# Performance work log

Hardware: AMD Instinct MI355X
Metric: run time of the kernel (lower is better)

The kernel has to match this reference:

```python
import jax, jax.numpy as jnp
from jax import lax
import numpy as np

RADIUS = 0.1
NSAMPLE = 32
STRIDE = 4
NUM_DIR = 32
BN_EPS = 1e-5


def _fps(p, m):
    # furthest point sampling: p (B,N,3) -> (B,m) int32 indices, start at index 0
    B, N, _ = p.shape

    def step(carry, _):
        dists, last = carry
        lp = jnp.take_along_axis(p, jnp.broadcast_to(last[:, None, None], (B, 1, 3)), axis=1)
        d = jnp.sum((p - lp) ** 2, axis=-1)
        dists = jnp.minimum(dists, d)
        nxt = jnp.argmax(dists, axis=-1).astype(jnp.int32)
        return (dists, nxt), nxt

    last0 = jnp.zeros((B,), jnp.int32)
    d0 = jnp.full((B, N), 1e10, p.dtype)
    _, rest = lax.scan(step, (d0, last0), None, length=m - 1)
    return jnp.concatenate([last0[None, :], rest], axis=0).T  # (B, m)


def _ball_query(q, p, k, radius):
    # q (B,M,3) centers, p (B,N,3) support -> (B,M,k) indices of first k points in ball,
    # padded with the first found index (PointNet++ convention)
    N = p.shape[1]
    d2 = jnp.sum((q[:, :, None, :] - p[:, None, :, :]) ** 2, axis=-1)  # (B,M,N)
    cand = jnp.where(d2 < radius * radius, jnp.arange(N, dtype=jnp.int32), N)
    cand = jnp.sort(cand, axis=-1)[:, :, :k]
    first = cand[:, :, :1]
    return jnp.where(cand == N, first, cand)


def _bn(x, g, b, m, v):
    # BatchNorm1d eval mode on (B,C,N)
    return (x - m[:, None]) * (g[:, None] / jnp.sqrt(v[:, None] + BN_EPS)) + b[:, None]


def _normalize(x, axis):
    return x / jnp.maximum(jnp.linalg.norm(x, axis=axis, keepdims=True), 1e-12)


def setup_inputs() -> dict:
    key = jax.random.key(0)
    ks = jax.random.split(key, 16)
    B, N, Cin, Cout = 4, 8192, 128, 256
    half = Cout // 2
    s = 0.02
    return {
        "p": jax.random.uniform(ks[0], (B, N, 3), jnp.float32),
        "f": jax.random.normal(ks[1], (B, Cin, N), jnp.float32),
        "conv1_w": jax.random.normal(ks[2], (Cout, Cin), jnp.float32) * s,
        "conv1_b": jax.random.normal(ks[3], (Cout,), jnp.float32) * s,
        "skip_w": jax.random.normal(ks[4], (Cout, Cin), jnp.float32) * s,
        "skip_b": jax.random.normal(ks[5], (Cout,), jnp.float32) * s,
        "bn1_g": jnp.ones((Cout,), jnp.float32),
        "bn1_b": jnp.zeros((Cout,), jnp.float32),
        "bn1_m": jax.random.normal(ks[6], (Cout,), jnp.float32) * 0.1,
        "bn1_v": jax.random.uniform(ks[7], (Cout,), jnp.float32) + 0.5,
        "dir_vectors": jax.random.normal(ks[8], (NUM_DIR, 3), jnp.float32),
        "de_w1": jax.random.normal(ks[9], (half, NUM_DIR), jnp.float32) * s,
        "de_g": jnp.ones((half,), jnp.float32),
        "de_bb": jnp.zeros((half,), jnp.float32),
        "de_m": jax.random.normal(ks[10], (half,), jnp.float32) * 0.1,
        "de_v": jax.random.uniform(ks[11], (half,), jnp.float32) + 0.5,
        "de_w2": jax.random.normal(ks[12], (Cout, half), jnp.float32) * s,
        "de_b2": jax.random.normal(ks[13], (Cout,), jnp.float32) * s,
    }


def reference(p, f, conv1_w, conv1_b, skip_w, skip_b, bn1_g, bn1_b, bn1_m, bn1_v,
              dir_vectors, de_w1, de_g, de_bb, de_m, de_v, de_w2, de_b2):
    B, N, _ = p.shape
    Cout = conv1_w.shape[0]
    M, K = N // STRIDE, NSAMPLE

    # FPS sampling + centroid gather
    idx = _fps(p, M)  # (B,M)
    new_p = jnp.take_along_axis(p, jnp.broadcast_to(idx[:, :, None], (B, M, 3)), axis=1)

    # residual branch: gather input feats at centroids, 1x1 conv (bn_after=False)
    fi = jnp.take_along_axis(f, jnp.broadcast_to(idx[:, None, :], (B, f.shape[1], M)), axis=2)
    identity = jnp.einsum('oc,bcm->bom', skip_w, fi) + skip_b[:, None]

    # convs1: 1x1 conv on all N points
    f1 = jnp.einsum('oc,bcn->bon', conv1_w, f) + conv1_b[:, None]  # (B,Cout,N)

    # ball-query grouping
    qidx = _ball_query(new_p, p, K, RADIUS)  # (B,M,K)
    idxf = qidx.reshape(B, M * K)
    gp = jnp.take_along_axis(p, jnp.broadcast_to(idxf[:, :, None], (B, M * K, 3)), axis=1).reshape(B, M, K, 3)
    dp = jnp.transpose(gp - new_p[:, :, None, :], (0, 3, 1, 2))  # (B,3,M,K)
    fj = jnp.take_along_axis(f1, jnp.broadcast_to(idxf[:, None, :], (B, Cout, M * K)), axis=2).reshape(B, Cout, M, K)

    # directional encoding
    dpn = _normalize(dp, axis=1)
    vec = _normalize(dir_vectors, axis=1)  # (NUM_DIR,3)
    theta = jnp.einsum('md,bdnk->bmnk', vec, dpn)  # (B,NUM_DIR,M,K)
    tmax = theta.max(axis=-1)  # (B,NUM_DIR,M)
    h = jnp.einsum('om,bmn->bon', de_w1, tmax)
    h = jax.nn.gelu(_bn(h, de_g, de_bb, de_m, de_v), approximate=False)
    pe = jnp.einsum('oc,bcn->bon', de_w2, h) + de_b2[:, None]

    # neighbor max-pool + BN + residuals
    f_out = _bn(fj.max(axis=-1), bn1_g, bn1_b, bn1_m, bn1_v) + pe + identity
    return new_p, f_out
```

## Files before the change

kernel.cpp:

```cpp
#include <hip/hip_runtime.h>

#define BATCH 4
#define NPTS 8192
#define MPTS 2048
#define CIN 128
#define CO 256
#define KS 32
#define ND 32
#define HALF 128

typedef unsigned int u32;
typedef unsigned long long u64;
typedef float f32x2 __attribute__((ext_vector_type(2)));

#define DPPC_QUAD_XOR1 0xB1
#define DPPC_QUAD_XOR2 0x4E
#define DPPC_ROW_MIRROR 0x140
#define DPPC_ROW_HALF_MIRROR 0x141
#define DPPC_ROW_BCAST15 0x142
#define DPPC_ROW_BCAST31 0x143

template<int CTRL>
__device__ __forceinline__ float dpp_max(float v) {
    int o = __builtin_amdgcn_update_dpp(__float_as_int(-1e30f), __float_as_int(v),
                                        CTRL, 0xF, 0xF, false);
    return fmaxf(v, __int_as_float(o));
}
__device__ __forceinline__ float wave_max_f32(float v) {
    v = dpp_max<DPPC_QUAD_XOR1>(v);
    v = dpp_max<DPPC_QUAD_XOR2>(v);
    v = dpp_max<DPPC_ROW_HALF_MIRROR>(v);
    v = dpp_max<DPPC_ROW_MIRROR>(v);
    v = dpp_max<DPPC_ROW_BCAST15>(v);
    v = dpp_max<DPPC_ROW_BCAST31>(v);
    return __int_as_float(__builtin_amdgcn_readlane(__float_as_int(v), 63));
}

__device__ __forceinline__ f32x2 pk_add(f32x2 a, f32x2 b) {
    f32x2 r;
    asm("v_pk_add_f32 %0, %1, %2" : "=v"(r) : "v"(a), "v"(b));
    return r;
}
__device__ __forceinline__ f32x2 pk_mul(f32x2 a, f32x2 b) {
    f32x2 r;
    asm("v_pk_mul_f32 %0, %1, %2" : "=v"(r) : "v"(a), "v"(b));
    return r;
}

struct FeatSmem {
    float sdx[KS], sdy[KS], sdz[KS];
    float ltm[ND], lfi[CIN], lh[HALF];
    int swidx[4][KS];
    int scnt[4];
    int nb[KS], nbp[KS];
};

__global__
__attribute__((amdgpu_flat_work_group_size(512, 512), amdgpu_waves_per_eu(2, 2)))
void k_mega(
    const float* __restrict__ p, const float* __restrict__ f,
    const float* __restrict__ conv1_w, const float* __restrict__ conv1_b,
    const float* __restrict__ skip_w,  const float* __restrict__ skip_b,
    const float* __restrict__ bn1_g, const float* __restrict__ bn1_b,
    const float* __restrict__ bn1_m, const float* __restrict__ bn1_v,
    const float* __restrict__ dirv,  const float* __restrict__ de_w1,
    const float* __restrict__ de_g,  const float* __restrict__ de_bb,
    const float* __restrict__ de_m,  const float* __restrict__ de_v,
    const float* __restrict__ de_w2, const float* __restrict__ de_b2,
    float* __restrict__ out_newp, float* __restrict__ out_f,
    int* __restrict__ idx, float* __restrict__ f1t,
    int* prog, int* f1all) {
    __shared__ __align__(16) char smem_u[16640];
    if (blockIdx.x < 4) {
        u64*    wkey = (u64*)smem_u;
        float4* wxyz = (float4*)(smem_u + 128);
        int b = blockIdx.x, t = threadIdx.x;
        int lane = t & 63, wid = t >> 6;
        int j0 = t * 16;
        const float* pb = p + (size_t)b * NPTS * 3;
        const float* pt = pb + t * 48;
        float px[16], py[16], pz[16];
#pragma unroll
        for (int c = 0; c < 4; ++c) {
            float4 q0 = *(const float4*)(pt + c * 12 + 0);
            float4 q1 = *(const float4*)(pt + c * 12 + 4);
            float4 q2 = *(const float4*)(pt + c * 12 + 8);
            px[c*4+0] = q0.x; py[c*4+0] = q0.y; pz[c*4+0] = q0.z;
            px[c*4+1] = q0.w; py[c*4+1] = q1.x; pz[c*4+1] = q1.y;
            px[c*4+2] = q1.z; py[c*4+2] = q1.w; pz[c*4+2] = q2.x;
            px[c*4+3] = q2.y; py[c*4+3] = q2.z; pz[c*4+3] = q2.w;
        }
        f32x2 px2[8], py2[8], pz2[8], dist2[8];
#pragma unroll
        for (int i = 0; i < 8; ++i) {
            px2[i].x = px[2*i]; px2[i].y = px[2*i+1];
            py2[i].x = py[2*i]; py2[i].y = py[2*i+1];
            pz2[i].x = pz[2*i]; pz2[i].y = pz[2*i+1];
        }
#pragma unroll
        for (int i = 0; i < 8; ++i) {
            asm volatile("" : "+v"(px2[i]), "+v"(py2[i]), "+v"(pz2[i]));
        }
#pragma unroll
        for (int i = 0; i < 8; ++i) { dist2[i].x = 1e10f; dist2[i].y = 1e10f; }
        float lx = pb[0], ly = pb[1], lz = pb[2];
        if (t == 0) {
            out_newp[(size_t)b * MPTS * 3 + 0] = lx;
            out_newp[(size_t)b * MPTS * 3 + 1] = ly;
            out_newp[(size_t)b * MPTS * 3 + 2] = lz;
            __hip_atomic_store(idx + b * MPTS, 0, __ATOMIC_RELAXED,
                               __HIP_MEMORY_SCOPE_AGENT);
        }
        for (int s = 1; s < MPTS; ++s) {
            int par = s & 1;
            f32x2 nlx2, nly2, nlz2;
            nlx2.x = -lx; nlx2.y = -lx;
            nly2.x = -ly; nly2.y = -ly;
            nlz2.x = -lz; nlz2.y = -lz;
            float bv = -1e30f; int bi = 0;
            float bx = px2[0].x, by = py2[0].x, bz = pz2[0].x;
#pragma unroll
            for (int i = 0; i < 8; ++i) {
                f32x2 dx = pk_add(px2[i], nlx2);
                f32x2 dy = pk_add(py2[i], nly2);
                f32x2 dz = pk_add(pz2[i], nlz2);
                f32x2 d  = pk_add(pk_add(pk_mul(dx, dx), pk_mul(dy, dy)),
                                  pk_mul(dz, dz));
                float nd0 = fminf(dist2[i].x, d.x);
                float nd1 = fminf(dist2[i].y, d.y);
                dist2[i].x = nd0;
                dist2[i].y = nd1;
                bool g0 = nd0 > bv;
                bi = g0 ? 2*i : bi;
                bx = g0 ? px2[i].x : bx;
                by = g0 ? py2[i].x : by;
                bz = g0 ? pz2[i].x : bz;
                bv = fmaxf(bv, nd0);
                bool g1 = nd1 > bv;
                bi = g1 ? 2*i+1 : bi;
                bx = g1 ? px2[i].y : bx;
                by = g1 ? py2[i].y : by;
                bz = g1 ? pz2[i].y : bz;
                bv = fmaxf(bv, nd1);
            }
            float gmw = wave_max_f32(bv);
            u64 mask = __ballot(bv == gmw);
            int first = __ffsll((long long)mask) - 1;
            if (lane == first) {
                wkey[par * 8 + wid] = ((u64)__float_as_uint(gmw) << 32)
                                    | (u64)(u32)(NPTS - 1 - (j0 + bi));
                wxyz[par * 8 + wid] = make_float4(bx, by, bz, 0.0f);
            }
            __syncthreads();
            const u64* wk = wkey + par * 8;
            u64 k0 = wk[0], k1 = wk[1], k2 = wk[2], k3 = wk[3];
            u64 k4 = wk[4], k5 = wk[5], k6 = wk[6], k7 = wk[7];
            u64 m01 = k1 > k0 ? k1 : k0;  int w01 = k1 > k0 ? 1 : 0;
            u64 m23 = k3 > k2 ? k3 : k2;  int w23 = k3 > k2 ? 3 : 2;
            u64 m45 = k5 > k4 ? k5 : k4;  int w45 = k5 > k4 ? 5 : 4;
            u64 m67 = k7 > k6 ? k7 : k6;  int w67 = k7 > k6 ? 7 : 6;
            u64 m03 = m23 > m01 ? m23 : m01; int w03 = m23 > m01 ? w23 : w01;
            u64 m47 = m67 > m45 ? m67 : m45; int w47 = m67 > m45 ? w67 : w45;
            u64 best = m47 > m03 ? m47 : m03; int ww = m47 > m03 ? w47 : w03;
            float4 wp = wxyz[par * 8 + ww];
            lx = wp.x; ly = wp.y; lz = wp.z;
            if (t == 0) {
                int w0 = (NPTS - 1 - (int)(best & 0xFFFFFFFFull)) & (NPTS - 1);
                asm volatile("s_waitcnt vmcnt(0)" ::: "memory");
                __hip_atomic_store(prog + b, s, __ATOMIC_RELAXED,
                                   __HIP_MEMORY_SCOPE_AGENT);
                out_newp[((size_t)b * MPTS + s) * 3 + 0] = lx;
                out_newp[((size_t)b * MPTS + s) * 3 + 1] = ly;
                out_newp[((size_t)b * MPTS + s) * 3 + 2] = lz;
                __hip_atomic_store(idx + b * MPTS + s, w0, __ATOMIC_RELAXED,
                                   __HIP_MEMORY_SCOPE_AGENT);
            }
        }
        if (t == 0) {
            asm volatile("s_waitcnt vmcnt(0)" ::: "memory");
            __hip_atomic_store(prog + b, MPTS, __ATOMIC_RELAXED,
                               __HIP_MEMORY_SCOPE_AGENT);
        }
    } else if (blockIdx.x < 4 + 1024) {
        float* fT = (float*)smem_u;
        int blk = blockIdx.x - 4;
        int b = blk >> 8;
        int n0 = (blk & 255) << 5;
        int t = threadIdx.x;
        const float* fb = f + (size_t)b * CIN * NPTS;
        for (int e = t; e < CIN * 32; e += 512) {
            int k = e >> 5, j = e & 31;
            fT[e] = fb[(size_t)k * NPTS + n0 + j];
        }
        __syncthreads();
        int c = t & 255, jh = (t >> 8) << 4;
        float bias = conv1_b[c];
        float acc[16];
#pragma unroll
        for (int j = 0; j < 16; ++j) acc[j] = bias;
        const float4* wrow4 = (const float4*)(conv1_w + (size_t)c * CIN);
        const float4* fT4 = (const float4*)fT;
        for (int k4 = 0; k4 < 32; ++k4) {
            float4 wv = wrow4[k4];
#pragma unroll
            for (int sub = 0; sub < 4; ++sub) {
                float w = sub == 0 ? wv.x : sub == 1 ? wv.y : sub == 2 ? wv.z : wv.w;
                int k = k4 * 4 + sub;
                int base = (k * 32 + jh) >> 2;
                float4 a0 = fT4[base+0], a1 = fT4[base+1], a2 = fT4[base+2], a3 = fT4[base+3];
                acc[0]  = fmaf(w, a0.x, acc[0]);  acc[1]  = fmaf(w, a0.y, acc[1]);
                acc[2]  = fmaf(w, a0.z, acc[2]);  acc[3]  = fmaf(w, a0.w, acc[3]);
                acc[4]  = fmaf(w, a1.x, acc[4]);  acc[5]  = fmaf(w, a1.y, acc[5]);
                acc[6]  = fmaf(w, a1.z, acc[6]);  acc[7]  = fmaf(w, a1.w, acc[7]);
                acc[8]  = fmaf(w, a2.x, acc[8]);  acc[9]  = fmaf(w, a2.y, acc[9]);
                acc[10] = fmaf(w, a2.z, acc[10]); acc[11] = fmaf(w, a2.w, acc[11]);
                acc[12] = fmaf(w, a3.x, acc[12]); acc[13] = fmaf(w, a3.y, acc[13]);
                acc[14] = fmaf(w, a3.z, acc[14]); acc[15] = fmaf(w, a3.w, acc[15]);
            }
        }
        float* dst = f1t + ((size_t)b * NPTS + n0 + jh) * CO + c;
#pragma unroll
        for (int j = 0; j < 16; ++j) dst[(size_t)j * CO] = acc[j];
        __syncthreads();
        if (t == 0) {
            __threadfence();
            atomicAdd(f1all, 1);
        }
    } else {
        int fb = (int)blockIdx.x - (4 + 1024);
        int m  = fb >> 1;
        int bA = (fb & 1) * 2;
        int t = threadIdx.x;
        if (t == 0) {
            int need = m + 1;
            for (int it = 0; it < (1 << 21); ++it) {
                if (__hip_atomic_load(prog + bA, __ATOMIC_RELAXED,
                                      __HIP_MEMORY_SCOPE_AGENT) >= need) break;
                __builtin_amdgcn_s_sleep(127);
            }
            for (int it = 0; it < (1 << 21); ++it) {
                if (__hip_atomic_load(prog + bA + 1, __ATOMIC_RELAXED,
                                      __HIP_MEMORY_SCOPE_AGENT) >= need) break;
                __builtin_amdgcn_s_sleep(127);
            }
            for (int it = 0; it < (1 << 21); ++it) {
                if (__hip_atomic_load(f1all, __ATOMIC_RELAXED,
                                      __HIP_MEMORY_SCOPE_AGENT) >= 1024) break;
                __builtin_amdgcn_s_sleep(127);
            }
            (void)__hip_atomic_load(prog + bA, __ATOMIC_ACQUIRE,
                                    __HIP_MEMORY_SCOPE_AGENT);
        }
        __syncthreads();
        int qi = t >> 8;
        int tq = t & 255;
        int b  = bA + qi;
        FeatSmem* fs = ((FeatSmem*)smem_u) + qi;
        int lane = t & 63, wq = (t >> 6) & 3;
        const float* pb = p + (size_t)b * NPTS * 3;
        int i0 = idx[(size_t)b * MPTS + m] & (NPTS - 1);
        float qx = pb[i0 * 3 + 0], qy = pb[i0 * 3 + 1], qz = pb[i0 * 3 + 2];
        const float R2 = 0.1f * 0.1f;

        int cnt = 0;
        int seg = wq * 2048;
        for (int base = 0; base < 2048; base += 64) {
            int j = seg + base + lane;
            float dx = __fsub_rn(pb[j * 3 + 0], qx);
            float dy = __fsub_rn(pb[j * 3 + 1], qy);
            float dz = __fsub_rn(pb[j * 3 + 2], qz);
            float d2 = __fadd_rn(__fadd_rn(__fmul_rn(dx, dx), __fmul_rn(dy, dy)),
                                 __fmul_rn(dz, dz));
            bool hit = d2 < R2;
            u64 mask = __ballot(hit);
            if (hit) {
                int pos = cnt + __popcll(mask & ((1ull << lane) - 1ull));
                if (pos < KS) fs->swidx[wq][pos] = j;
            }
            cnt += __popcll(mask);
            if (cnt >= KS) break;
        }
        if (lane == 0) fs->scnt[wq] = cnt < KS ? cnt : KS;
        __syncthreads();
        int c0s = fs->scnt[0], c1s = fs->scnt[1], c2s = fs->scnt[2], c3s = fs->scnt[3];
        int st1 = c0s, st2 = c0s + c1s, st3 = c0s + c1s + c2s;
        int total = c0s + c1s + c2s + c3s; if (total > KS) total = KS;
        if (total < 1) total = 1;
        if (tq < 128) {
            int ww = tq >> 5, l = tq & 31;
            int stw = (ww == 0) ? 0 : (ww == 1) ? st1 : (ww == 2) ? st2 : st3;
            int cw  = (ww == 0) ? c0s : (ww == 1) ? c1s : (ww == 2) ? c2s : c3s;
            int gp = stw + l;
            if (l < cw && gp < KS) fs->nb[gp] = fs->swidx[ww][l];
        }
        __syncthreads();
        if (tq < KS) {
            int jk = fs->nb[tq < total ? tq : 0] & (NPTS - 1);
            fs->nbp[tq] = jk;
            float dx = pb[jk * 3 + 0] - qx;
            float dy = pb[jk * 3 + 1] - qy;
            float dz = pb[jk * 3 + 2] - qz;
            float nr = fmaxf(sqrtf(dx * dx + dy * dy + dz * dz), 1e-12f);
            fs->sdx[tq] = dx / nr; fs->sdy[tq] = dy / nr; fs->sdz[tq] = dz / nr;
        }
        if (tq >= 128) {
            fs->lfi[tq - 128] = f[((size_t)b * CIN + (tq - 128)) * NPTS + i0];
        }
        __syncthreads();
        if (tq < ND) {
            float ax = dirv[tq * 3], ay = dirv[tq * 3 + 1], az = dirv[tq * 3 + 2];
            float n = fmaxf(sqrtf(ax * ax + ay * ay + az * az), 1e-12f);
            float vx = ax / n, vy = ay / n, vz = az / n;
            float tm = -1e30f;
#pragma unroll
            for (int k = 0; k < KS; ++k)
                tm = fmaxf(tm, vx * fs->sdx[k] + vy * fs->sdy[k] + vz * fs->sdz[k]);
            fs->ltm[tq] = tm;
        }
        __syncthreads();

        int c = tq;
        const float* f1b = f1t + (size_t)b * NPTS * CO + c;
        float mx = -1e30f;
#pragma unroll 8
        for (int k = 0; k < KS; ++k) {
            mx = fmaxf(mx, f1b[(size_t)fs->nbp[k] * CO]);
        }
        float sc1 = bn1_g[c] / sqrtf(bn1_v[c] + 1e-5f);
        float o1 = (mx - bn1_m[c]) * sc1 + bn1_b[c];

        float idv = skip_b[c];
        {
            const float4* sr = (const float4*)(skip_w + (size_t)c * CIN);
#pragma unroll 8
            for (int r = 0; r < 32; ++r) {
                float4 v = sr[r];
                idv = fmaf(v.x, fs->lfi[r*4+0], fmaf(v.y, fs->lfi[r*4+1],
                      fmaf(v.z, fs->lfi[r*4+2], fmaf(v.w, fs->lfi[r*4+3], idv))));
            }
        }
        {
            int hc = c & (HALF - 1);
            const float4* d1 = (const float4*)(de_w1 + (size_t)hc * ND);
            float a = 0.0f;
#pragma unroll
            for (int r = 0; r < 8; ++r) {
                float4 v = d1[r];
                a = fmaf(v.x, fs->ltm[r*4+0], fmaf(v.y, fs->ltm[r*4+1],
                    fmaf(v.z, fs->ltm[r*4+2], fmaf(v.w, fs->ltm[r*4+3], a))));
            }
            float dsc = de_g[hc] / sqrtf(de_v[hc] + 1e-5f);
            float xb = (a - de_m[hc]) * dsc + de_bb[hc];
            float hv = 0.5f * xb * (1.0f + erff(xb * 0.70710678118654752440f));
            if (c < HALF) fs->lh[c] = hv;
        }
        __syncthreads();
        float pe = de_b2[c];
        {
            const float4* d2p = (const float4*)(de_w2 + (size_t)c * HALF);
#pragma unroll 8
            for (int r = 0; r < 32; ++r) {
                float4 v = d2p[r];
                pe = fmaf(v.x, fs->lh[r*4+0], fmaf(v.y, fs->lh[r*4+1],
                     fmaf(v.z, fs->lh[r*4+2], fmaf(v.w, fs->lh[r*4+3], pe))));
            }
        }
        out_f[((size_t)b * CO + c) * MPTS + m] = o1 + pe + idv;
    }
}

__global__ __launch_bounds__(512, 2) void k_fps_f1(
    const float* __restrict__ p, const float* __restrict__ f,
    const float* __restrict__ conv1_w, const float* __restrict__ conv1_b,
    float* __restrict__ out_newp, int* __restrict__ idx,
    float* __restrict__ f1t) {
    __shared__ __align__(16) char smem_u[33024];
    if (blockIdx.x < 4) {
        u64*   wkey = (u64*)smem_u;
        int*   sidx = (int*)(smem_u + 128);
        float* sx   = (float*)(smem_u + 128 + 4 * MPTS);
        float* sy   = sx + MPTS;
        float* sz   = sy + MPTS;
        int b = blockIdx.x, t = threadIdx.x;
        int lane = t & 63, wid = t >> 6;
        int j0 = t * 16;
        const float* pb = p + (size_t)b * NPTS * 3;
        const float* pt = pb + t * 48;
        float px[16], py[16], pz[16], dist[16];
#pragma unroll
        for (int c = 0; c < 4; ++c) {
            float4 q0 = *(const float4*)(pt + c * 12 + 0);
            float4 q1 = *(const float4*)(pt + c * 12 + 4);
            float4 q2 = *(const float4*)(pt + c * 12 + 8);
            px[c*4+0] = q0.x; py[c*4+0] = q0.y; pz[c*4+0] = q0.z;
            px[c*4+1] = q0.w; py[c*4+1] = q1.x; pz[c*4+1] = q1.y;
            px[c*4+2] = q1.z; py[c*4+2] = q1.w; pz[c*4+2] = q2.x;
            px[c*4+3] = q2.y; py[c*4+3] = q2.z; pz[c*4+3] = q2.w;
        }
#pragma unroll
        for (int i = 0; i < 16; ++i) dist[i] = 1e10f;
        float lx = pb[0], ly = pb[1], lz = pb[2];
        if (t == 0) { sidx[0] = 0; sx[0] = lx; sy[0] = ly; sz[0] = lz; }
        for (int s = 1; s < MPTS; ++s) {
            int par = s & 1;
            float bv = -1e30f; int bi = 0;
#pragma unroll
            for (int i = 0; i < 16; ++i) {
                float dx = __fsub_rn(px[i], lx);
                float dy = __fsub_rn(py[i], ly);
                float dz = __fsub_rn(pz[i], lz);
                float d  = __fadd_rn(__fadd_rn(__fmul_rn(dx, dx), __fmul_rn(dy, dy)),
                                     __fmul_rn(dz, dz));
                float nd = fminf(dist[i], d);
                dist[i] = nd;
                bool gt = nd > bv;
                bi = gt ? i : bi;
                bv = fmaxf(bv, nd);
            }
            float gmw = wave_max_f32(bv);
            u64 mask = __ballot(bv == gmw);
            int first = __ffsll((long long)mask) - 1;
            if (lane == first) {
                wkey[par * 8 + wid] = ((u64)__float_as_uint(gmw) << 32)
                                    | (u64)(u32)(NPTS - 1 - (j0 + bi));
            }
            __syncthreads();
            const u64* wk = wkey + par * 8;
            u64 k0 = wk[0], k1 = wk[1], k2 = wk[2], k3 = wk[3];
            u64 k4 = wk[4], k5 = wk[5], k6 = wk[6], k7 = wk[7];
            u64 m01 = k1 > k0 ? k1 : k0;
            u64 m23 = k3 > k2 ? k3 : k2;
            u64 m45 = k5 > k4 ? k5 : k4;
            u64 m67 = k7 > k6 ? k7 : k6;
            u64 m03 = m23 > m01 ? m23 : m01;
            u64 m47 = m67 > m45 ? m67 : m45;
            u64 best = m47 > m03 ? m47 : m03;
            int w0 = (NPTS - 1 - (int)(best & 0xFFFFFFFFull)) & (NPTS - 1);
            int w0s = __builtin_amdgcn_readfirstlane(w0);
            lx = pb[w0s * 3 + 0]; ly = pb[w0s * 3 + 1]; lz = pb[w0s * 3 + 2];
            if (t == 0) { sidx[s] = w0s; sx[s] = lx; sy[s] = ly; sz[s] = lz; }
        }
        __syncthreads();
        for (int e = t; e < MPTS; e += 512) {
            int base = (b * MPTS + e) * 3;
            out_newp[base + 0] = sx[e];
            out_newp[base + 1] = sy[e];
            out_newp[base + 2] = sz[e];
            idx[b * MPTS + e] = sidx[e];
        }
    } else if (f1t != nullptr) {
        float* fT = (float*)smem_u;
        int blk = blockIdx.x - 4;
        int b = blk >> 8;
        int n0 = (blk & 255) << 5;
        int t = threadIdx.x;
        const float* fb = f + (size_t)b * CIN * NPTS;
        for (int e = t; e < CIN * 32; e += 512) {
            int k = e >> 5, j = e & 31;
            fT[e] = fb[(size_t)k * NPTS + n0 + j];
        }
        __syncthreads();
        int c = t & 255, jh = (t >> 8) << 4;
        float bias = conv1_b[c];
        float acc[16];
#pragma unroll
        for (int j = 0; j < 16; ++j) acc[j] = bias;
        const float4* wrow4 = (const float4*)(conv1_w + (size_t)c * CIN);
        const float4* fT4 = (const float4*)fT;
        for (int k4 = 0; k4 < 32; ++k4) {
            float4 wv = wrow4[k4];
#pragma unroll
            for (int sub = 0; sub < 4; ++sub) {
                float w = sub == 0 ? wv.x : sub == 1 ? wv.y : sub == 2 ? wv.z : wv.w;
                int k = k4 * 4 + sub;
                int base = (k * 32 + jh) >> 2;
                float4 a0 = fT4[base+0], a1 = fT4[base+1], a2 = fT4[base+2], a3 = fT4[base+3];
                acc[0]  = fmaf(w, a0.x, acc[0]);  acc[1]  = fmaf(w, a0.y, acc[1]);
                acc[2]  = fmaf(w, a0.z, acc[2]);  acc[3]  = fmaf(w, a0.w, acc[3]);
                acc[4]  = fmaf(w, a1.x, acc[4]);  acc[5]  = fmaf(w, a1.y, acc[5]);
                acc[6]  = fmaf(w, a1.z, acc[6]);  acc[7]  = fmaf(w, a1.w, acc[7]);
                acc[8]  = fmaf(w, a2.x, acc[8]);  acc[9]  = fmaf(w, a2.y, acc[9]);
                acc[10] = fmaf(w, a2.z, acc[10]); acc[11] = fmaf(w, a2.w, acc[11]);
                acc[12] = fmaf(w, a3.x, acc[12]); acc[13] = fmaf(w, a3.y, acc[13]);
                acc[14] = fmaf(w, a3.z, acc[14]); acc[15] = fmaf(w, a3.w, acc[15]);
            }
        }
        float* dst = f1t + ((size_t)b * NPTS + n0 + jh) * CO + c;
#pragma unroll
        for (int j = 0; j < 16; ++j) dst[(size_t)j * CO] = acc[j];
    }
}

__global__ __launch_bounds__(256) void k_f1(const float* __restrict__ f,
                                            const float* __restrict__ conv1_w,
                                            const float* __restrict__ conv1_b,
                                            float* __restrict__ f1t, int b0) {
    __shared__ __align__(16) float fT[CIN * 16];
    int blk = blockIdx.x;
    int bl = blk >> 9;
    int b = b0 + bl;
    int n0 = (blk & 511) << 4;
    int t = threadIdx.x;
    const float* fb = f + (size_t)b * CIN * NPTS;
    for (int e = t; e < CIN * 16; e += 256) {
        int k = e >> 4, j = e & 15;
        fT[e] = fb[(size_t)k * NPTS + n0 + j];
    }
    __syncthreads();
    int c = t;
    float bias = conv1_b[c];
    float acc[16];
#pragma unroll
    for (int j = 0; j < 16; ++j) acc[j] = bias;
    const float4* wrow4 = (const float4*)(conv1_w + (size_t)c * CIN);
    const float4* fT4 = (const float4*)fT;
    for (int k4 = 0; k4 < 32; ++k4) {
        float4 wv = wrow4[k4];
#pragma unroll
        for (int sub = 0; sub < 4; ++sub) {
            float w = sub == 0 ? wv.x : sub == 1 ? wv.y : sub == 2 ? wv.z : wv.w;
            int k = k4 * 4 + sub;
            float4 a0 = fT4[k*4+0], a1 = fT4[k*4+1], a2 = fT4[k*4+2], a3 = fT4[k*4+3];
            acc[0]  = fmaf(w, a0.x, acc[0]);  acc[1]  = fmaf(w, a0.y, acc[1]);
            acc[2]  = fmaf(w, a0.z, acc[2]);  acc[3]  = fmaf(w, a0.w, acc[3]);
            acc[4]  = fmaf(w, a1.x, acc[4]);  acc[5]  = fmaf(w, a1.y, acc[5]);
            acc[6]  = fmaf(w, a1.z, acc[6]);  acc[7]  = fmaf(w, a1.w, acc[7]);
            acc[8]  = fmaf(w, a2.x, acc[8]);  acc[9]  = fmaf(w, a2.y, acc[9]);
            acc[10] = fmaf(w, a2.z, acc[10]); acc[11] = fmaf(w, a2.w, acc[11]);
            acc[12] = fmaf(w, a3.x, acc[12]); acc[13] = fmaf(w, a3.y, acc[13]);
            acc[14] = fmaf(w, a3.z, acc[14]); acc[15] = fmaf(w, a3.w, acc[15]);
        }
    }
    float* dst = f1t + ((size_t)bl * NPTS + n0) * CO + c;
#pragma unroll
    for (int j = 0; j < 16; ++j) dst[(size_t)j * CO] = acc[j];
}

__global__ __launch_bounds__(256) void k_feat(
    const float* __restrict__ p, const float* __restrict__ f,
    const float* __restrict__ f1t,
    const float* __restrict__ skip_w,  const float* __restrict__ skip_b,
    const float* __restrict__ bn1_g, const float* __restrict__ bn1_b,
    const float* __restrict__ bn1_m, const float* __restrict__ bn1_v,
    const float* __restrict__ dirv,  const float* __restrict__ de_w1,
    const float* __restrict__ de_g,  const float* __restrict__ de_bb,
    const float* __restrict__ de_m,  const float* __restrict__ de_v,
    const float* __restrict__ de_w2, const float* __restrict__ de_b2,
    const int* __restrict__ idx,     float* __restrict__ out_f, int b0) {
    __shared__ float sdx[KS], sdy[KS], sdz[KS];
    __shared__ float ltm[ND], lfi[CIN], lh[HALF];
    __shared__ int swidx[4][KS];
    __shared__ int scnt[4];
    __shared__ int nb[KS], nbp[KS];

    int q = b0 * MPTS + blockIdx.x;
    int b = q >> 11;
    int bl = b - b0;
    int m = q & (MPTS - 1);
    int t = threadIdx.x, lane = t & 63, w = t >> 6;
    const float* pb = p + (size_t)b * NPTS * 3;
    int i0 = idx[q] & (NPTS - 1);
    float qx = pb[i0 * 3 + 0], qy = pb[i0 * 3 + 1], qz = pb[i0 * 3 + 2];
    const float R2 = 0.1f * 0.1f;

    int cnt = 0;
    int seg = w * 2048;
    for (int base = 0; base < 2048; base += 64) {
        int j = seg + base + lane;
        float dx = __fsub_rn(pb[j * 3 + 0], qx);
        float dy = __fsub_rn(pb[j * 3 + 1], qy);
        float dz = __fsub_rn(pb[j * 3 + 2], qz);
        float d2 = __fadd_rn(__fadd_rn(__fmul_rn(dx, dx), __fmul_rn(dy, dy)),
                             __fmul_rn(dz, dz));
        bool hit = d2 < R2;
        u64 mask = __ballot(hit);
        if (hit) {
            int pos = cnt + __popcll(mask & ((1ull << lane) - 1ull));
            if (pos < KS) swidx[w][pos] = j;
        }
        cnt += __popcll(mask);
        if (cnt >= KS) break;
    }
    if (lane == 0) scnt[w] = cnt < KS ? cnt : KS;
    __syncthreads();
    int c0s = scnt[0], c1s = scnt[1], c2s = scnt[2], c3s = scnt[3];
    int st1 = c0s, st2 = c0s + c1s, st3 = c0s + c1s + c2s;
    int total = c0s + c1s + c2s + c3s; if (total > KS) total = KS;
    if (total < 1) total = 1;
    if (t < 128) {
        int ww = t >> 5, l = t & 31;
        int stw = (ww == 0) ? 0 : (ww == 1) ? st1 : (ww == 2) ? st2 : st3;
        int cw  = (ww == 0) ? c0s : (ww == 1) ? c1s : (ww == 2) ? c2s : c3s;
        int gp = stw + l;
        if (l < cw && gp < KS) nb[gp] = swidx[ww][l];
    }
    __syncthreads();
    if (t < KS) {
        int jk = nb[t < total ? t : 0] & (NPTS - 1);
        nbp[t] = jk;
        float dx = pb[jk * 3 + 0] - qx;
        float dy = pb[jk * 3 + 1] - qy;
        float dz = pb[jk * 3 + 2] - qz;
        float nr = fmaxf(sqrtf(dx * dx + dy * dy + dz * dz), 1e-12f);
        sdx[t] = dx / nr; sdy[t] = dy / nr; sdz[t] = dz / nr;
    }
    if (t >= 128) {
        lfi[t - 128] = f[((size_t)b * CIN + (t - 128)) * NPTS + i0];
    }
    __syncthreads();
    if (t < ND) {
        float ax = dirv[t * 3], ay = dirv[t * 3 + 1], az = dirv[t * 3 + 2];
        float n = fmaxf(sqrtf(ax * ax + ay * ay + az * az), 1e-12f);
        float vx = ax / n, vy = ay / n, vz = az / n;
        float tm = -1e30f;
#pragma unroll
        for (int k = 0; k < KS; ++k)
            tm = fmaxf(tm, vx * sdx[k] + vy * sdy[k] + vz * sdz[k]);
        ltm[t] = tm;
    }
    __syncthreads();

    int c = t;
    const float* f1b = f1t + (size_t)bl * NPTS * CO + c;
    float mx = -1e30f;
#pragma unroll 8
    for (int k = 0; k < KS; ++k) {
        mx = fmaxf(mx, f1b[(size_t)nbp[k] * CO]);
    }
    float sc1 = bn1_g[c] / sqrtf(bn1_v[c] + 1e-5f);
    float o1 = (mx - bn1_m[c]) * sc1 + bn1_b[c];

    float idv = skip_b[c];
    {
        const float4* sr = (const float4*)(skip_w + (size_t)c * CIN);
#pragma unroll 8
        for (int r = 0; r < 32; ++r) {
            float4 v = sr[r];
            idv = fmaf(v.x, lfi[r*4+0], fmaf(v.y, lfi[r*4+1],
                  fmaf(v.z, lfi[r*4+2], fmaf(v.w, lfi[r*4+3], idv))));
        }
    }
    {
        int hc = c & (HALF - 1);
        const float4* d1 = (const float4*)(de_w1 + (size_t)hc * ND);
        float a = 0.0f;
#pragma unroll
        for (int r = 0; r < 8; ++r) {
            float4 v = d1[r];
            a = fmaf(v.x, ltm[r*4+0], fmaf(v.y, ltm[r*4+1],
                fmaf(v.z, ltm[r*4+2], fmaf(v.w, ltm[r*4+3], a))));
        }
        float dsc = de_g[hc] / sqrtf(de_v[hc] + 1e-5f);
        float xb = (a - de_m[hc]) * dsc + de_bb[hc];
        float hv = 0.5f * xb * (1.0f + erff(xb * 0.70710678118654752440f));
        if (c < HALF) lh[c] = hv;
    }
    __syncthreads();
    float pe = de_b2[c];
    {
        const float4* d2p = (const float4*)(de_w2 + (size_t)c * HALF);
#pragma unroll 8
        for (int r = 0; r < 32; ++r) {
            float4 v = d2p[r];
            pe = fmaf(v.x, lh[r*4+0], fmaf(v.y, lh[r*4+1],
                 fmaf(v.z, lh[r*4+2], fmaf(v.w, lh[r*4+3], pe))));
        }
    }
    out_f[((size_t)b * CO + c) * MPTS + m] = o1 + pe + idv;
}

__global__ __launch_bounds__(256) void k_featz_fused(
    const float* __restrict__ p, const float* __restrict__ f,
    const float* __restrict__ conv1_w, const float* __restrict__ conv1_b,
    const float* __restrict__ skip_w,  const float* __restrict__ skip_b,
    const float* __restrict__ bn1_g, const float* __restrict__ bn1_b,
    const float* __restrict__ bn1_m, const float* __restrict__ bn1_v,
    const float* __restrict__ dirv,  const float* __restrict__ de_w1,
    const float* __restrict__ de_g,  const float* __restrict__ de_bb,
    const float* __restrict__ de_m,  const float* __restrict__ de_v,
    const float* __restrict__ de_w2, const float* __restrict__ de_b2,
    const int* __restrict__ idx,     float* __restrict__ out_f) {
    __shared__ __align__(16) float fg[KS * CIN];
    __shared__ float sdx[KS], sdy[KS], sdz[KS];
    __shared__ float ltm[ND], lfi[CIN], lh[HALF];
    __shared__ int swidx[4][KS];
    __shared__ int scnt[4];
    __shared__ int nb[KS], nbp[KS];

    int q = blockIdx.x;
    int b = q >> 11;
    int m = q & (MPTS - 1);
    int t = threadIdx.x, lane = t & 63, w = t >> 6;
    const float* pb = p + (size_t)b * NPTS * 3;
    int i0 = idx[q] & (NPTS - 1);
    float qx = pb[i0 * 3 + 0], qy = pb[i0 * 3 + 1], qz = pb[i0 * 3 + 2];
    const float R2 = 0.1f * 0.1f;
    int cnt = 0;
    int seg = w * 2048;
    for (int base = 0; base < 2048; base += 64) {
        int j = seg + base + lane;
        float dx = __fsub_rn(pb[j * 3 + 0], qx);
        float dy = __fsub_rn(pb[j * 3 + 1], qy);
        float dz = __fsub_rn(pb[j * 3 + 2], qz);
        float d2 = __fadd_rn(__fadd_rn(__fmul_rn(dx, dx), __fmul_rn(dy, dy)),
                             __fmul_rn(dz, dz));
        bool hit = d2 < R2;
        u64 mask = __ballot(hit);
        if (hit) {
            int pos = cnt + __popcll(mask & ((1ull << lane) - 1ull));
            if (pos < KS) swidx[w][pos] = j;
        }
        cnt += __popcll(mask);
        if (cnt >= KS) break;
    }
    if (lane == 0) scnt[w] = cnt < KS ? cnt : KS;
    __syncthreads();
    int c0s = scnt[0], c1s = scnt[1], c2s = scnt[2], c3s = scnt[3];
    int st1 = c0s, st2 = c0s + c1s, st3 = c0s + c1s + c2s;
    int total = c0s + c1s + c2s + c3s; if (total > KS) total = KS;
    if (total < 1) total = 1;
    if (t < 128) {
        int ww = t >> 5, l = t & 31;
        int stw = (ww == 0) ? 0 : (ww == 1) ? st1 : (ww == 2) ? st2 : st3;
        int cw  = (ww == 0) ? c0s : (ww == 1) ? c1s : (ww == 2) ? c2s : c3s;
        int gp = stw + l;
        if (l < cw && gp < KS) nb[gp] = swidx[ww][l];
    }
    __syncthreads();
    if (t < KS) {
        int jk = nb[t < total ? t : 0] & (NPTS - 1);
        nbp[t] = jk;
        float dx = pb[jk * 3 + 0] - qx;
        float dy = pb[jk * 3 + 1] - qy;
        float dz = pb[jk * 3 + 2] - qz;
        float nr = fmaxf(sqrtf(dx * dx + dy * dy + dz * dz), 1e-12f);
        sdx[t] = dx / nr; sdy[t] = dy / nr; sdz[t] = dz / nr;
    }
    if (t >= 128) lfi[t - 128] = f[((size_t)b * CIN + (t - 128)) * NPTS + i0];
    __syncthreads();
    if (t < ND) {
        float ax = dirv[t * 3], ay = dirv[t * 3 + 1], az = dirv[t * 3 + 2];
        float n = fmaxf(sqrtf(ax * ax + ay * ay + az * az), 1e-12f);
        float vx = ax / n, vy = ay / n, vz = az / n;
        float tm = -1e30f;
#pragma unroll
        for (int k = 0; k < KS; ++k)
            tm = fmaxf(tm, vx * sdx[k] + vy * sdy[k] + vz * sdz[k]);
        ltm[t] = tm;
    }
    for (int e = t; e < KS * CIN; e += 256) {
        int k = e >> 7, i = e & 127;
        fg[k * CIN + i] = f[((size_t)b * CIN + i) * NPTS + nbp[k]];
    }
    __syncthreads();
    int c = t;
    float acc[KS];
#pragma unroll
    for (int k = 0; k < KS; ++k) acc[k] = 0.0f;
    const float4* w4 = (const float4*)(conv1_w + (size_t)c * CIN);
    const float4* fg4 = (const float4*)fg;
    for (int i4 = 0; i4 < 32; ++i4) {
        float4 wv = w4[i4];
#pragma unroll 8
        for (int k = 0; k < KS; ++k) {
            float4 g = fg4[k * 32 + i4];
            acc[k] = fmaf(wv.x, g.x, fmaf(wv.y, g.y,
                     fmaf(wv.z, g.z, fmaf(wv.w, g.w, acc[k]))));
        }
    }
    float bias = conv1_b[c];
    float mx = -1e30f;
#pragma unroll
    for (int k = 0; k < KS; ++k) mx = fmaxf(mx, acc[k] + bias);
    float sc1 = bn1_g[c] / sqrtf(bn1_v[c] + 1e-5f);
    float o1 = (mx - bn1_m[c]) * sc1 + bn1_b[c];
    float idv = skip_b[c];
    {
        const float4* sr = (const float4*)(skip_w + (size_t)c * CIN);
#pragma unroll 8
        for (int r = 0; r < 32; ++r) {
            float4 v = sr[r];
            idv = fmaf(v.x, lfi[r*4+0], fmaf(v.y, lfi[r*4+1],
                  fmaf(v.z, lfi[r*4+2], fmaf(v.w, lfi[r*4+3], idv))));
        }
    }
    {
        int hc = c & (HALF - 1);
        const float4* d1 = (const float4*)(de_w1 + (size_t)hc * ND);
        float a = 0.0f;
#pragma unroll
        for (int r = 0; r < 8; ++r) {
            float4 v = d1[r];
            a = fmaf(v.x, ltm[r*4+0], fmaf(v.y, ltm[r*4+1],
                fmaf(v.z, ltm[r*4+2], fmaf(v.w, ltm[r*4+3], a))));
        }
        float dsc = de_g[hc] / sqrtf(de_v[hc] + 1e-5f);
        float xb = (a - de_m[hc]) * dsc + de_bb[hc];
        float hv = 0.5f * xb * (1.0f + erff(xb * 0.70710678118654752440f));
        if (c < HALF) lh[c] = hv;
    }
    __syncthreads();
    float pe = de_b2[c];
    {
        const float4* d2p = (const float4*)(de_w2 + (size_t)c * HALF);
#pragma unroll 8
        for (int r = 0; r < 32; ++r) {
            float4 v = d2p[r];
            pe = fmaf(v.x, lh[r*4+0], fmaf(v.y, lh[r*4+1],
                 fmaf(v.z, lh[r*4+2], fmaf(v.w, lh[r*4+3], pe))));
        }
    }
    out_f[((size_t)b * CO + c) * MPTS + m] = o1 + pe + idv;
}

extern "C" void kernel_launch(void* const* d_in, const int* in_sizes, int n_in,
                              void* d_out, int out_size, void* d_ws, size_t ws_size,
                              hipStream_t stream) {
    const float* p       = (const float*)d_in[0];
    const float* f       = (const float*)d_in[1];
    const float* conv1_w = (const float*)d_in[2];
    const float* conv1_b = (const float*)d_in[3];
    const float* skip_w  = (const float*)d_in[4];
    const float* skip_b  = (const float*)d_in[5];
    const float* bn1_g   = (const float*)d_in[6];
    const float* bn1_b   = (const float*)d_in[7];
    const float* bn1_m   = (const float*)d_in[8];
    const float* bn1_v   = (const float*)d_in[9];
    const float* dirv    = (const float*)d_in[10];
    const float* de_w1   = (const float*)d_in[11];
    const float* de_g    = (const float*)d_in[12];
    const float* de_bb   = (const float*)d_in[13];
    const float* de_m    = (const float*)d_in[14];
    const float* de_v    = (const float*)d_in[15];
    const float* de_w2   = (const float*)d_in[16];
    const float* de_b2   = (const float*)d_in[17];

    float* out_newp = (float*)d_out;
    float* out_f    = (float*)d_out + (size_t)BATCH * MPTS * 3;
    int*   idx      = (int*)d_ws;

    size_t f1_one  = (size_t)NPTS * CO * 4;
    size_t need_stream = 32768 + 128 + 4 * f1_one;
    size_t need_full   = 32768 + 4 * f1_one;
    size_t need_one    = 32768 + f1_one;

    if (ws_size >= need_stream) {
        int*   prog  = (int*)((char*)d_ws + 32768);
        int*   f1all = prog + 4;
        float* f1t   = (float*)((char*)d_ws + 32768 + 128);
        hipMemsetAsync(prog, 0, 128, stream);
        k_mega<<<dim3(4 + 1024 + 4096), dim3(512), 0, stream>>>(
            p, f, conv1_w, conv1_b, skip_w, skip_b, bn1_g, bn1_b, bn1_m, bn1_v,
            dirv, de_w1, de_g, de_bb, de_m, de_v, de_w2, de_b2,
            out_newp, out_f, idx, f1t, prog, f1all);
    } else if (ws_size >= need_full) {
        float* f1t = (float*)((char*)d_ws + 32768);
        k_fps_f1<<<dim3(4 + 1024), dim3(512), 0, stream>>>(
            p, f, conv1_w, conv1_b, out_newp, idx, f1t);
        k_feat<<<dim3(4 * MPTS), dim3(256), 0, stream>>>(
            p, f, f1t, skip_w, skip_b, bn1_g, bn1_b, bn1_m, bn1_v,
            dirv, de_w1, de_g, de_bb, de_m, de_v, de_w2, de_b2, idx, out_f, 0);
    } else if (ws_size >= need_one) {
        float* f1t = (float*)((char*)d_ws + 32768);
        k_fps_f1<<<dim3(4), dim3(512), 0, stream>>>(
            p, f, conv1_w, conv1_b, out_newp, idx, nullptr);
        for (int b0 = 0; b0 < BATCH; ++b0) {
            k_f1  <<<dim3(512),  dim3(256), 0, stream>>>(f, conv1_w, conv1_b, f1t, b0);
            k_feat<<<dim3(MPTS), dim3(256), 0, stream>>>(
                p, f, f1t, skip_w, skip_b, bn1_g, bn1_b, bn1_m, bn1_v,
                dirv, de_w1, de_g, de_bb, de_m, de_v, de_w2, de_b2, idx, out_f, b0);
        }
    } else {
        k_fps_f1<<<dim3(4), dim3(512), 0, stream>>>(
            p, f, conv1_w, conv1_b, out_newp, idx, nullptr);
        k_featz_fused<<<dim3(BATCH * MPTS), dim3(256), 0, stream>>>(
            p, f, conv1_w, conv1_b, skip_w, skip_b, bn1_g, bn1_b, bn1_m, bn1_v,
            dirv, de_w1, de_g, de_bb, de_m, de_v, de_w2, de_b2, idx, out_f);
    }
}
```

Measured before the change: 2.507 ms.

## Replace per-step FPS block barrier with tagged LDS spin-wait handoff

The serial furthest-point-sampling loop ran a __syncthreads on every one of its 2047 steps so waves could exchange their per-wave argmax. Now each wave stamps its packed key with a 16-bit step tag in a dedicated double-buffered LDS array. The other waves spin on volatile reads until all 8 tags match, instead of waiting at a full workgroup barrier. This aims to cut barrier latency on the serial critical path, at the cost of LDS polling traffic and reliance on the ordering between the coordinate write and the key write.

Result: slower. 3.303 ms (+31.8%).

```diff
diff --git a/kernel.cpp b/kernel.cpp
--- a/kernel.cpp
+++ b/kernel.cpp
@@ -71,9 +71,9 @@
     int* __restrict__ idx, float* __restrict__ f1t,
     int* prog, int* f1all) {
     __shared__ __align__(16) char smem_u[16640];
+    __shared__ __align__(16) u64    wkey[2][8];
+    __shared__ __align__(16) float4 wxyz[2][8];
     if (blockIdx.x < 4) {
-        u64*    wkey = (u64*)smem_u;
-        float4* wxyz = (float4*)(smem_u + 128);
         int b = blockIdx.x, t = threadIdx.x;
         int lane = t & 63, wid = t >> 6;
         int j0 = t * 16;
@@ -104,6 +104,7 @@
 #pragma unroll
         for (int i = 0; i < 8; ++i) { dist2[i].x = 1e10f; dist2[i].y = 1e10f; }
         float lx = pb[0], ly = pb[1], lz = pb[2];
+        if (t < 16) ((u64*)wkey)[t] = (u64)0xFFFFull << 16;
         if (t == 0) {
             out_newp[(size_t)b * MPTS * 3 + 0] = lx;
             out_newp[(size_t)b * MPTS * 3 + 1] = ly;
@@ -111,8 +112,10 @@
             __hip_atomic_store(idx + b * MPTS, 0, __ATOMIC_RELAXED,
                                __HIP_MEMORY_SCOPE_AGENT);
         }
+        __syncthreads();
         for (int s = 1; s < MPTS; ++s) {
             int par = s & 1;
+            u32 tag = (u32)s & 0xFFFFu;
             f32x2 nlx2, nly2, nlz2;
             nlx2.x = -lx; nlx2.y = -lx;
             nly2.x = -ly; nly2.y = -ly;
@@ -147,14 +150,28 @@
             u64 mask = __ballot(bv == gmw);
             int first = __ffsll((long long)mask) - 1;
             if (lane == first) {
-                wkey[par * 8 + wid] = ((u64)__float_as_uint(gmw) << 32)
-                                    | (u64)(u32)(NPTS - 1 - (j0 + bi));
-                wxyz[par * 8 + wid] = make_float4(bx, by, bz, 0.0f);
-            }
-            __syncthreads();
-            const u64* wk = wkey + par * 8;
-            u64 k0 = wk[0], k1 = wk[1], k2 = wk[2], k3 = wk[3];
-            u64 k4 = wk[4], k5 = wk[5], k6 = wk[6], k7 = wk[7];
+                wxyz[par][wid] = make_float4(bx, by, bz, 0.0f);
+                asm volatile("s_waitcnt lgkmcnt(0)" ::: "memory");
+                u64 key = ((u64)__float_as_uint(gmw) << 32)
+                        | ((u64)tag << 16)
+                        | (u64)(u32)(NPTS - 1 - (j0 + bi));
+                *(volatile u64*)&wkey[par][wid] = key;
+            }
+            volatile u64* wk = (volatile u64*)wkey[par];
+            u64 k0, k1, k2, k3, k4, k5, k6, k7;
+            for (int it = 0; it < (1 << 20); ++it) {
+                k0 = wk[0]; k1 = wk[1]; k2 = wk[2]; k3 = wk[3];
+                k4 = wk[4]; k5 = wk[5]; k6 = wk[6]; k7 = wk[7];
+                u32 agg = ((u32)(k0 >> 16) & 0xFFFFu) ^ tag;
+                agg |= ((u32)(k1 >> 16) & 0xFFFFu) ^ tag;
+                agg |= ((u32)(k2 >> 16) & 0xFFFFu) ^ tag;
+                agg |= ((u32)(k3 >> 16) & 0xFFFFu) ^ tag;
+                agg |= ((u32)(k4 >> 16) & 0xFFFFu) ^ tag;
+                agg |= ((u32)(k5 >> 16) & 0xFFFFu) ^ tag;
+                agg |= ((u32)(k6 >> 16) & 0xFFFFu) ^ tag;
+                agg |= ((u32)(k7 >> 16) & 0xFFFFu) ^ tag;
+                if (agg == 0u) break;
+            }
             u64 m01 = k1 > k0 ? k1 : k0;  int w01 = k1 > k0 ? 1 : 0;
             u64 m23 = k3 > k2 ? k3 : k2;  int w23 = k3 > k2 ? 3 : 2;
             u64 m45 = k5 > k4 ? k5 : k4;  int w45 = k5 > k4 ? 5 : 4;
@@ -162,10 +179,10 @@
             u64 m03 = m23 > m01 ? m23 : m01; int w03 = m23 > m01 ? w23 : w01;
             u64 m47 = m67 > m45 ? m67 : m45; int w47 = m67 > m45 ? w67 : w45;
             u64 best = m47 > m03 ? m47 : m03; int ww = m47 > m03 ? w47 : w03;
-            float4 wp = wxyz[par * 8 + ww];
+            float4 wp = wxyz[par][ww];
             lx = wp.x; ly = wp.y; lz = wp.z;
             if (t == 0) {
-                int w0 = (NPTS - 1 - (int)(best & 0xFFFFFFFFull)) & (NPTS - 1);
+                int w0 = (NPTS - 1 - (int)(best & 0xFFFFull)) & (NPTS - 1);
                 asm volatile("s_waitcnt vmcnt(0)" ::: "memory");
                 __hip_atomic_store(prog + b, s, __ATOMIC_RELAXED,
                                    __HIP_MEMORY_SCOPE_AGENT);
```
